# Performance work log

Measured on AMD Instinct MI355X. Metric: run time of the kernel, lower is better.

The kernel has to match this reference:

```python
import jax, jax.numpy as jnp
import numpy as np

HIDDEN = 512
HEADS = 8
HEAD_DIM = HIDDEN // HEADS
EPS_LN = 1e-5
EPS_ATTN = 1e-6


def setup_inputs() -> dict:
    key = jax.random.key(0)
    ks = jax.random.split(key, 12)
    B, S, N, D = 4, 12, 2048, HIDDEN
    s = 1.0 / np.sqrt(D)
    x = jax.random.normal(ks[0], (B, S, N, D), dtype=jnp.float32)
    Wq = jax.random.normal(ks[1], (D, D), dtype=jnp.float32) * s
    bq = jnp.zeros((D,), dtype=jnp.float32)
    Wk = jax.random.normal(ks[2], (D, D), dtype=jnp.float32) * s
    bk = jnp.zeros((D,), dtype=jnp.float32)
    Wv = jax.random.normal(ks[3], (D, D), dtype=jnp.float32) * s
    bv = jnp.zeros((D,), dtype=jnp.float32)
    Wo = jax.random.normal(ks[4], (D, D), dtype=jnp.float32) * s
    bo = jnp.zeros((D,), dtype=jnp.float32)
    ln_g = jnp.ones((D,), dtype=jnp.float32)
    ln_b = jnp.zeros((D,), dtype=jnp.float32)
    return {"x": x, "Wq": Wq, "bq": bq, "Wk": Wk, "bk": bk,
            "Wv": Wv, "bv": bv, "Wo": Wo, "bo": bo,
            "ln_g": ln_g, "ln_b": ln_b}


def _layer_norm(x, g, b):
    mu = jnp.mean(x, axis=-1, keepdims=True)
    var = jnp.var(x, axis=-1, keepdims=True)
    return (x - mu) * jax.lax.rsqrt(var + EPS_LN) * g + b


def reference(x, Wq, bq, Wk, bk, Wv, bv, Wo, bo, ln_g, ln_b):
    B, S, N, D = x.shape
    L = S * N  # flattened spatiotemporal tokens
    residual = x
    h = _layer_norm(x, ln_g, ln_b).reshape(B, L, D)
    # projections; [B, L, D] -> [B, H, L, hd]
    def split_heads(t):
        return t.reshape(B, L, HEADS, HEAD_DIM).transpose(0, 2, 1, 3)
    q = split_heads(h @ Wq.T + bq)
    k = split_heads(h @ Wk.T + bk)
    v = split_heads(h @ Wv.T + bv)
    # elu+1 feature map
    q = jax.nn.elu(q) + 1.0
    k = jax.nn.elu(k) + 1.0
    # kv outer product: [B, H, hd, hd]
    kv = jnp.einsum('bhld,bhle->bhde', k, v)
    out = jnp.einsum('bhld,bhde->bhle', q, kv)
    normalizer = jnp.einsum('bhld,bhd->bhl', q, k.sum(axis=2))
    out = out / (normalizer[..., None] + EPS_ATTN)
    out = out.transpose(0, 2, 1, 3).reshape(B, L, D)
    out = out @ Wo.T + bo
    out = out.reshape(B, S, N, D)
    return out + residual
```

## Files before the change

### kernel.cpp

```cpp
#include <hip/hip_runtime.h>
#include <hip/hip_bf16.h>
#include <stdint.h>

#define DDIM 512
#define NHEAD 8
#define BATCH 4
#define LTOK 24576
#define MROWS 98304
#define QKV_MBLK 384
#define KVCH 96
#define OG_MBLK 768
#define OG_MBLK_B 192
#define PTILE 4160

typedef __attribute__((ext_vector_type(8))) short short8;
typedef __attribute__((ext_vector_type(4))) float f32x4;

__device__ __forceinline__ float bf2f(unsigned short u) {
  union { unsigned int i; float f; } c; c.i = ((unsigned int)u) << 16; return c.f;
}
__device__ __forceinline__ unsigned short f2bf(float f) {
  __hip_bfloat16 h = __float2bfloat16(f);
  return __builtin_bit_cast(unsigned short, h);
}
__device__ __forceinline__ void gload16(const void* g, void* l) {
  __builtin_amdgcn_global_load_lds((const __attribute__((address_space(1))) void*)g,
                                   (__attribute__((address_space(3))) void*)l, 16, 0, 0);
}
__device__ __forceinline__ float elu1(float v) { return (v > 0.f) ? (v + 1.f) : __expf(v); }

__global__ __launch_bounds__(256) void wprep(const float* __restrict__ Wq, const float* __restrict__ bq,
                                             const float* __restrict__ Wk, const float* __restrict__ bk,
                                             const float* __restrict__ Wv, const float* __restrict__ bv,
                                             const float* __restrict__ Wo,
                                             unsigned short* __restrict__ wf,
                                             unsigned short* __restrict__ wob,
                                             float* __restrict__ biasf) {
  long t = (long)blockIdx.x * 256 + threadIdx.x;
  if (t < 786432) {
    int f = (int)(t >> 9), c = (int)(t & 511);
    const float* src;
    if (f < 1024) { int hh = f >> 7, kv = (f >> 6) & 1, d = f & 63;
                    src = (kv ? Wv : Wk) + (long)(hh * 64 + d) * 512; }
    else          src = Wq + (long)(f - 1024) * 512;
    wf[t] = f2bf(src[c]);
  } else if (t < 786432 + 262144) {
    long i = t - 786432; wob[i] = f2bf(Wo[i]);
  } else if (t < 786432 + 262144 + 1536) {
    int f = (int)(t - (786432 + 262144));
    float v;
    if (f < 1024) { int hh = f >> 7, kv = (f >> 6) & 1, d = f & 63; v = (kv ? bv : bk)[hh * 64 + d]; }
    else v = bq[f - 1024];
    biasf[f] = v;
  }
}

__global__ __launch_bounds__(256) void ln_kernel(const float* __restrict__ x,
                                                 const float* __restrict__ g,
                                                 const float* __restrict__ b,
                                                 unsigned short* __restrict__ h) {
  int wv = threadIdx.x >> 6, lane = threadIdx.x & 63;
  long row = (long)blockIdx.x * 4 + wv;
  const float* xr = x + row * DDIM + lane * 8;
  float4 v0 = *(const float4*)xr;
  float4 v1 = *(const float4*)(xr + 4);
  float s  = v0.x + v0.y + v0.z + v0.w + v1.x + v1.y + v1.z + v1.w;
  float s2 = v0.x*v0.x + v0.y*v0.y + v0.z*v0.z + v0.w*v0.w
           + v1.x*v1.x + v1.y*v1.y + v1.z*v1.z + v1.w*v1.w;
  #pragma unroll
  for (int o = 32; o; o >>= 1) { s += __shfl_xor(s, o); s2 += __shfl_xor(s2, o); }
  float mu = s * (1.0f / DDIM);
  float var = s2 * (1.0f / DDIM) - mu * mu;
  float rs = rsqrtf(var + 1e-5f);
  float4 g0 = *(const float4*)(g + lane * 8);
  float4 g1 = *(const float4*)(g + lane * 8 + 4);
  float4 b0 = *(const float4*)(b + lane * 8);
  float4 b1 = *(const float4*)(b + lane * 8 + 4);
  short8 o;
  o[0] = (short)f2bf((v0.x - mu) * rs * g0.x + b0.x);
  o[1] = (short)f2bf((v0.y - mu) * rs * g0.y + b0.y);
  o[2] = (short)f2bf((v0.z - mu) * rs * g0.z + b0.z);
  o[3] = (short)f2bf((v0.w - mu) * rs * g0.w + b0.w);
  o[4] = (short)f2bf((v1.x - mu) * rs * g1.x + b1.x);
  o[5] = (short)f2bf((v1.y - mu) * rs * g1.y + b1.y);
  o[6] = (short)f2bf((v1.z - mu) * rs * g1.z + b1.z);
  o[7] = (short)f2bf((v1.w - mu) * rs * g1.w + b1.w);
  *(short8*)(h + row * DDIM + lane * 8) = o;
}

__device__ __forceinline__ short8 ldsfrag(const unsigned short* h, int row, int kg) {
  return *(const short8*)&h[row * 32 + ((kg ^ ((row >> 1) & 3)) << 3)];
}

__device__ __forceinline__ void stage_half(const unsigned short* gbase,
                                           unsigned short* ldsbase, int tid) {
  #pragma unroll
  for (int i = 0; i < 2; i++) {
    int c = i * 512 + tid;
    int rr = c >> 2, cc = c & 3;
    int sc = ((cc ^ ((rr >> 1) & 3)) << 3);
    gload16(gbase + (long)rr * DDIM + sc, ldsbase + c * 8);
  }
}

template <int VMP1, int VMP3, bool S01, bool S23>
__device__ __forceinline__ void ktile(int t, unsigned short* lds,
                                      const unsigned short* Ab, const unsigned short* Wb,
                                      f32x4 (&acc)[8][4],
                                      int wm, int wn, int lr, int kg, int tid) {
  const int buf = t & 1;
  unsigned short* A0l = lds + (buf * 2 + 0) * 8192;
  unsigned short* A1l = lds + (buf * 2 + 1) * 8192;
  unsigned short* B0l = lds + 32768 + (buf * 2 + 0) * 8192;
  unsigned short* B1l = lds + 32768 + (buf * 2 + 1) * 8192;
  unsigned short* A1n = lds + ((buf ^ 1) * 2 + 1) * 8192;
  unsigned short* B1n = lds + 32768 + ((buf ^ 1) * 2 + 1) * 8192;
  short8 a[4], b[4];

  #pragma unroll
  for (int m = 0; m < 4; m++) a[m] = ldsfrag(A0l, wm * 128 + m * 16 + lr, kg);
  #pragma unroll
  for (int n = 0; n < 4; n++) b[n] = ldsfrag(B0l, wn * 64 + n * 16 + lr, kg);
  if (S01) stage_half(Ab + (long)(t + 1) * 64 + 32, A1n, tid);
  __builtin_amdgcn_s_barrier();
  __builtin_amdgcn_s_setprio(1);
  #pragma unroll
  for (int m = 0; m < 4; m++)
    #pragma unroll
    for (int n = 0; n < 4; n++)
      acc[m][n] = __builtin_amdgcn_mfma_f32_16x16x32_bf16(a[m], b[n], acc[m][n], 0, 0, 0);
  __builtin_amdgcn_s_setprio(0);
  __builtin_amdgcn_s_barrier();
  __builtin_amdgcn_sched_barrier(0);

  #pragma unroll
  for (int m = 0; m < 4; m++) a[m] = ldsfrag(A0l, wm * 128 + (4 + m) * 16 + lr, kg);
  if (S01) stage_half(Wb + (long)(t + 1) * 64 + 32, B1n, tid);
  __builtin_amdgcn_s_barrier();
  __builtin_amdgcn_s_setprio(1);
  #pragma unroll
  for (int m = 0; m < 4; m++)
    #pragma unroll
    for (int n = 0; n < 4; n++)
      acc[4 + m][n] = __builtin_amdgcn_mfma_f32_16x16x32_bf16(a[m], b[n], acc[4 + m][n], 0, 0, 0);
  __builtin_amdgcn_s_setprio(0);
  asm volatile("s_waitcnt vmcnt(%0)" :: "i"(VMP1) : "memory");
  __builtin_amdgcn_s_barrier();
  __builtin_amdgcn_sched_barrier(0);

  #pragma unroll
  for (int m = 0; m < 4; m++) a[m] = ldsfrag(A1l, wm * 128 + m * 16 + lr, kg);
  #pragma unroll
  for (int n = 0; n < 4; n++) b[n] = ldsfrag(B1l, wn * 64 + n * 16 + lr, kg);
  if (S23) stage_half(Ab + (long)(t + 2) * 64, A0l, tid);
  __builtin_amdgcn_s_barrier();
  __builtin_amdgcn_s_setprio(1);
  #pragma unroll
  for (int m = 0; m < 4; m++)
    #pragma unroll
    for (int n = 0; n < 4; n++)
      acc[m][n] = __builtin_amdgcn_mfma_f32_16x16x32_bf16(a[m], b[n], acc[m][n], 0, 0, 0);
  __builtin_amdgcn_s_setprio(0);
  __builtin_amdgcn_s_barrier();
  __builtin_amdgcn_sched_barrier(0);

  #pragma unroll
  for (int m = 0; m < 4; m++) a[m] = ldsfrag(A1l, wm * 128 + (4 + m) * 16 + lr, kg);
  if (S23) stage_half(Wb + (long)(t + 2) * 64, B0l, tid);
  __builtin_amdgcn_s_barrier();
  __builtin_amdgcn_s_setprio(1);
  #pragma unroll
  for (int m = 0; m < 4; m++)
    #pragma unroll
    for (int n = 0; n < 4; n++)
      acc[4 + m][n] = __builtin_amdgcn_mfma_f32_16x16x32_bf16(a[m], b[n], acc[4 + m][n], 0, 0, 0);
  __builtin_amdgcn_s_setprio(0);
  asm volatile("s_waitcnt vmcnt(%0)" :: "i"(VMP3) : "memory");
  __builtin_amdgcn_s_barrier();
  __builtin_amdgcn_sched_barrier(0);
}

__global__ __launch_bounds__(512, 2) void qkv_gemm(const unsigned short* __restrict__ A,
                                                   const unsigned short* __restrict__ wf,
                                                   const float* __restrict__ biasf,
                                                   unsigned short* __restrict__ qbuf,
                                                   unsigned short* __restrict__ part) {
  __shared__ unsigned short lds[65536];

  int tid = threadIdx.x;
  int wv = tid >> 6, lane = tid & 63;
  int wm = wv >> 2, wn = wv & 3;
  int kg = lane >> 4, lr = lane & 15;

  int lin = blockIdx.x;
  int g = lin / 48, r = lin % 48;
  int xb = g * 8 + (r & 7);
  int y  = r >> 3;
  long mBase = (long)xb * 256;
  int nBase = y * 256;

  const unsigned short* Ab = A + mBase * DDIM;
  const unsigned short* Wb = wf + (long)nBase * DDIM;

  f32x4 acc[8][4];
  #pragma unroll
  for (int m = 0; m < 8; m++)
    #pragma unroll
    for (int n = 0; n < 4; n++) acc[m][n] = (f32x4){0.f, 0.f, 0.f, 0.f};

  stage_half(Ab,       lds + 0 * 8192, tid);
  stage_half(Wb,       lds + 32768 + 0 * 8192, tid);
  stage_half(Ab + 32,  lds + 1 * 8192, tid);
  stage_half(Wb + 32,  lds + 32768 + 1 * 8192, tid);
  stage_half(Ab + 64,  lds + 2 * 8192, tid);
  stage_half(Wb + 64,  lds + 32768 + 2 * 8192, tid);
  asm volatile("s_waitcnt vmcnt(8)" ::: "memory");
  __builtin_amdgcn_s_barrier();
  __builtin_amdgcn_sched_barrier(0);

  #pragma unroll 1
  for (int i = 0; i < 3; i++) {
    ktile<8, 8, true, true>(2 * i,     lds, Ab, Wb, acc, wm, wn, lr, kg, tid);
    ktile<8, 8, true, true>(2 * i + 1, lds, Ab, Wb, acc, wm, wn, lr, kg, tid);
  }
  ktile<8, 4, true, false>(6, lds, Ab, Wb, acc, wm, wn, lr, kg, tid);
  ktile<0, 63, false, false>(7, lds, Ab, Wb, acc, wm, wn, lr, kg, tid);

  __syncthreads();

  if (y < 4) {
    unsigned short* kT = lds;
    unsigned short* vT = lds + 16896;
    int batch = xb / KVCH;
    int cIdx  = xb % KVCH;

    {
      int rr = 64 + (tid >> 5), cc = tid & 31;
      short8 z;
      #pragma unroll
      for (int j = 0; j < 8; j++) z[j] = (rr == 64) ? (short)0x3F80 : (short)0;
      *(short8*)&vT[rr * 264 + cc * 8] = z;
    }

    #pragma unroll 1
    for (int p = 0; p < 2; p++) {
      if ((wn >> 1) == p) {
        bool isV = wn & 1;
        #pragma unroll
        for (int n = 0; n < 4; n++) {
          int feat = n * 16 + lr;
          float bv = biasf[nBase + wn * 64 + n * 16 + lr];
          #pragma unroll
          for (int m = 0; m < 8; m++)
            #pragma unroll
            for (int j = 0; j < 4; j++) {
              int tok = wm * 128 + m * 16 + kg * 4 + j;
              float v = acc[m][n][j] + bv;
              if (!isV) kT[feat * 264 + tok] = f2bf(elu1(v));
              else      vT[feat * 264 + tok] = f2bf(v);
            }
        }
      }
      __syncthreads();

      int mt = wv & 3, ngrp = wv >> 2;
      int h = y * 2 + p;
      long pbase = ((long)(batch * 8 + h) * KVCH + cIdx) * PTILE;
      if (!ngrp) {
        f32x4 pa0 = {0,0,0,0}, pa1 = {0,0,0,0}, pa2 = {0,0,0,0};
        #pragma unroll
        for (int kk = 0; kk < 8; kk++) {
          short8 af = *(const short8*)&kT[(mt * 16 + lr) * 264 + kk * 32 + kg * 8];
          short8 b0 = *(const short8*)&vT[(0 * 16 + lr) * 264 + kk * 32 + kg * 8];
          short8 b1 = *(const short8*)&vT[(1 * 16 + lr) * 264 + kk * 32 + kg * 8];
          short8 b2 = *(const short8*)&vT[(2 * 16 + lr) * 264 + kk * 32 + kg * 8];
          pa0 = __builtin_amdgcn_mfma_f32_16x16x32_bf16(af, b0, pa0, 0, 0, 0);
          pa1 = __builtin_amdgcn_mfma_f32_16x16x32_bf16(af, b1, pa1, 0, 0, 0);
          pa2 = __builtin_amdgcn_mfma_f32_16x16x32_bf16(af, b2, pa2, 0, 0, 0);
        }
        #pragma unroll
        for (int j = 0; j < 4; j++) {
          int d = mt * 16 + kg * 4 + j;
          part[pbase + d * 64 + (0 * 16 + lr)] = f2bf(pa0[j]);
          part[pbase + d * 64 + (1 * 16 + lr)] = f2bf(pa1[j]);
          part[pbase + d * 64 + (2 * 16 + lr)] = f2bf(pa2[j]);
        }
      } else {
        f32x4 pa0 = {0,0,0,0}, pa1 = {0,0,0,0};
        #pragma unroll
        for (int kk = 0; kk < 8; kk++) {
          short8 af = *(const short8*)&kT[(mt * 16 + lr) * 264 + kk * 32 + kg * 8];
          short8 b0 = *(const short8*)&vT[(3 * 16 + lr) * 264 + kk * 32 + kg * 8];
          short8 b1 = *(const short8*)&vT[(4 * 16 + lr) * 264 + kk * 32 + kg * 8];
          pa0 = __builtin_amdgcn_mfma_f32_16x16x32_bf16(af, b0, pa0, 0, 0, 0);
          pa1 = __builtin_amdgcn_mfma_f32_16x16x32_bf16(af, b1, pa1, 0, 0, 0);
        }
        #pragma unroll
        for (int j = 0; j < 4; j++) {
          int d = mt * 16 + kg * 4 + j;
          part[pbase + d * 64 + (3 * 16 + lr)] = f2bf(pa0[j]);
          if (lr == 0) part[pbase + 4096 + d] = f2bf(pa1[j]);
        }
      }
      __syncthreads();
    }
  } else {
    unsigned short* Cs = lds;
    int qc0 = (y - 4) * 256;
    #pragma unroll 1
    for (int half = 0; half < 2; half++) {
      if (wm == half) {
        #pragma unroll
        for (int n = 0; n < 4; n++) {
          int col = wn * 64 + n * 16 + lr;
          float bv = biasf[nBase + col];
          #pragma unroll
          for (int m = 0; m < 8; m++)
            #pragma unroll
            for (int j = 0; j < 4; j++) {
              int rowl = m * 16 + kg * 4 + j;
              Cs[rowl * 264 + col] = f2bf(elu1(acc[m][n][j] + bv));
            }
        }
      }
      __syncthreads();
      #pragma unroll
      for (int i = 0; i < 8; i++) {
        int idx = i * 512 + tid;
        int row = idx >> 5, ch = idx & 31;
        *(short8*)&qbuf[(mBase + half * 128 + row) * DDIM + qc0 + ch * 8] =
            *(const short8*)&Cs[row * 264 + ch * 8];
      }
      __syncthreads();
    }
  }
}

__global__ __launch_bounds__(256) void kv_final(const unsigned short* __restrict__ part,
                                                unsigned short* __restrict__ kvD,
                                                float* __restrict__ ksum) {
  int bh = blockIdx.x;
  int idx = blockIdx.y * 256 + threadIdx.x;
  if (idx >= PTILE) return;
  const unsigned short* base = part + (long)bh * KVCH * PTILE + idx;
  float s = 0.f;
  for (int c = 0; c < KVCH; c++) s += bf2f(base[(long)c * PTILE]);
  if (idx < 4096) kvD[bh * 4096 + idx] = f2bf(s);
  else            ksum[bh * 64 + (idx - 4096)] = s;
}

__global__ __launch_bounds__(512) void w2_gemm(const unsigned short* __restrict__ kvD,
                                               const unsigned short* __restrict__ wob,
                                               unsigned short* __restrict__ Bmat) {
  __shared__ unsigned short W2s[512 * 72];
  int t = threadIdx.x, wv = t >> 6, lane = t & 63;
  int kg = lane >> 4, lr = lane & 15;
  int bh = blockIdx.x, b = bh >> 3, h = bh & 7;
  const unsigned short* kva = kvD + bh * 4096;

  short8 a[4][2];
  #pragma unroll
  for (int m = 0; m < 4; m++)
    #pragma unroll
    for (int kk = 0; kk < 2; kk++)
      a[m][kk] = *(const short8*)&kva[(m * 16 + lr) * 64 + kk * 32 + kg * 8];

  f32x4 acc[4][4];
  #pragma unroll
  for (int m = 0; m < 4; m++)
    #pragma unroll
    for (int n = 0; n < 4; n++) acc[m][n] = (f32x4){0.f, 0.f, 0.f, 0.f};

  #pragma unroll
  for (int n = 0; n < 4; n++) {
    int c = wv * 64 + n * 16 + lr;
    #pragma unroll
    for (int kk = 0; kk < 2; kk++) {
      short8 bfr = *(const short8*)&wob[(long)c * 512 + h * 64 + kk * 32 + kg * 8];
      #pragma unroll
      for (int m = 0; m < 4; m++)
        acc[m][n] = __builtin_amdgcn_mfma_f32_16x16x32_bf16(a[m][kk], bfr, acc[m][n], 0, 0, 0);
    }
  }
  #pragma unroll
  for (int m = 0; m < 4; m++)
    #pragma unroll
    for (int n = 0; n < 4; n++)
      #pragma unroll
      for (int j = 0; j < 4; j++)
        W2s[(wv * 64 + n * 16 + lr) * 72 + m * 16 + kg * 4 + j] = f2bf(acc[m][n][j]);
  __syncthreads();
  #pragma unroll
  for (int pp = 0; pp < 8; pp++) {
    int idx = pp * 512 + t;
    int c = idx >> 3, ch = (idx & 7) * 8;
    *(short8*)&Bmat[(long)b * 262144 + (long)c * 512 + h * 64 + ch] =
        *(const short8*)&W2s[c * 72 + ch];
  }
}

__global__ __launch_bounds__(256) void qscale(unsigned short* __restrict__ q,
                                              const float* __restrict__ ksum) {
  int wv = threadIdx.x >> 6, lane = threadIdx.x & 63;
  long row = (long)blockIdx.x * 4 + wv;
  int batch = (int)(row / LTOK);
  int bh = batch * 8 + (lane >> 3);
  unsigned short* qr = q + row * DDIM + lane * 8;
  short8 qv = *(const short8*)qr;
  const float* ks = ksum + bh * 64 + (lane & 7) * 8;
  float4 k0 = *(const float4*)ks;
  float4 k1 = *(const float4*)(ks + 4);
  float qf[8];
  #pragma unroll
  for (int j = 0; j < 8; j++) qf[j] = bf2f((unsigned short)qv[j]);
  float n = qf[0]*k0.x + qf[1]*k0.y + qf[2]*k0.z + qf[3]*k0.w
          + qf[4]*k1.x + qf[5]*k1.y + qf[6]*k1.z + qf[7]*k1.w;
  n += __shfl_xor(n, 1);
  n += __shfl_xor(n, 2);
  n += __shfl_xor(n, 4);
  float s = 1.0f / (n + 1e-6f);
  short8 o;
  #pragma unroll
  for (int j = 0; j < 8; j++) o[j] = (short)f2bf(qf[j] * s);
  *(short8*)qr = o;
}

__global__ __launch_bounds__(256) void ogemm(const unsigned short* __restrict__ A,
                                             const unsigned short* __restrict__ Bm,
                                             const float* __restrict__ bo,
                                             const float* __restrict__ xres,
                                             float* __restrict__ out) {
  __shared__ union {
    struct { unsigned short As[128 * 64]; unsigned short Bs[128 * 64]; } st;
    float Cs[64 * 132];
  } sm;

  int t = threadIdx.x;
  int wv = t >> 6, lane = t & 63;
  int wm = wv >> 1, wn = wv & 1;
  int kg = lane >> 4, lr = lane & 15;

  int lin = blockIdx.x;
  int g = lin >> 5, r = lin & 31;
  int xb = g * 8 + (r & 7);
  int y  = r >> 3;
  long mBase = (long)xb * 128;
  int nBase = y * 128;
  int batch = xb / OG_MBLK_B;

  f32x4 acc[4][4];
  #pragma unroll
  for (int m = 0; m < 4; m++)
    #pragma unroll
    for (int n = 0; n < 4; n++) acc[m][n] = (f32x4){0.f, 0.f, 0.f, 0.f};

  const unsigned short* Ab = A + mBase * DDIM;
  const unsigned short* Bb = Bm + (long)batch * 262144 + (long)nBase * DDIM;

  for (int k0 = 0; k0 < DDIM; k0 += 64) {
    #pragma unroll
    for (int i = 0; i < 4; i++) {
      int c = i * 256 + t;
      int rr = c >> 3, cc = c & 7;
      int sc = ((cc ^ (rr & 7)) << 3);
      gload16(Ab + (long)rr * DDIM + k0 + sc, sm.st.As + c * 8);
      gload16(Bb + (long)rr * DDIM + k0 + sc, sm.st.Bs + c * 8);
    }
    __syncthreads();
    #pragma unroll
    for (int kk = 0; kk < 2; kk++) {
      short8 a[4], b[4];
      #pragma unroll
      for (int m = 0; m < 4; m++) {
        int row = wm * 64 + m * 16 + lr;
        a[m] = *(const short8*)&sm.st.As[row * 64 + (((kk * 4 + kg) ^ (row & 7)) << 3)];
      }
      #pragma unroll
      for (int n = 0; n < 4; n++) {
        int row = wn * 64 + n * 16 + lr;
        b[n] = *(const short8*)&sm.st.Bs[row * 64 + (((kk * 4 + kg) ^ (row & 7)) << 3)];
      }
      #pragma unroll
      for (int m = 0; m < 4; m++)
        #pragma unroll
        for (int n = 0; n < 4; n++)
          acc[m][n] = __builtin_amdgcn_mfma_f32_16x16x32_bf16(a[m], b[n], acc[m][n], 0, 0, 0);
    }
    __syncthreads();
  }

  for (int p = 0; p < 2; p++) {
    __syncthreads();
    if (wm == p) {
      #pragma unroll
      for (int n = 0; n < 4; n++) {
        int col = wn * 64 + n * 16 + lr;
        float bv = bo[nBase + col];
        #pragma unroll
        for (int m = 0; m < 4; m++)
          #pragma unroll
          for (int j = 0; j < 4; j++) {
            int lrow = m * 16 + kg * 4 + j;
            sm.Cs[lrow * 132 + col] = acc[m][n][j] + bv;
          }
      }
    }
    __syncthreads();
    #pragma unroll
    for (int pp = 0; pp < 8; pp++) {
      int idx = pp * 256 + t;
      int row = idx >> 5, c4 = idx & 31;
      long goff = (mBase + p * 64 + row) * DDIM + nBase + c4 * 4;
      float4 rv = *(const float4*)&xres[goff];
      float4 cv = *(const float4*)&sm.Cs[row * 132 + c4 * 4];
      float4 ov; ov.x = cv.x + rv.x; ov.y = cv.y + rv.y; ov.z = cv.z + rv.z; ov.w = cv.w + rv.w;
      *(float4*)&out[goff] = ov;
    }
  }
}

extern "C" void kernel_launch(void* const* d_in, const int* in_sizes, int n_in,
                              void* d_out, int out_size, void* d_ws, size_t ws_size,
                              hipStream_t stream) {
  const float* x    = (const float*)d_in[0];
  const float* Wq   = (const float*)d_in[1];
  const float* bq   = (const float*)d_in[2];
  const float* Wk   = (const float*)d_in[3];
  const float* bk   = (const float*)d_in[4];
  const float* Wv   = (const float*)d_in[5];
  const float* bv   = (const float*)d_in[6];
  const float* Wo   = (const float*)d_in[7];
  const float* bo   = (const float*)d_in[8];
  const float* ln_g = (const float*)d_in[9];
  const float* ln_b = (const float*)d_in[10];

  char* ws = (char*)d_ws;
  size_t SZ = (size_t)MROWS * DDIM * 2;
  unsigned short* hbuf = (unsigned short*)ws;
  unsigned short* qbuf = (unsigned short*)(ws + SZ);
  char* p = ws + 2 * SZ;
  unsigned short* wf   = (unsigned short*)p;  p += (size_t)1536 * 512 * 2;
  unsigned short* wob  = (unsigned short*)p;  p += (size_t)512 * 512 * 2;
  float* biasf         = (float*)p;           p += 1536 * 4;
  p = (char*)(((uintptr_t)p + 255) & ~(uintptr_t)255);
  unsigned short* part = (unsigned short*)p;  p += (size_t)32 * KVCH * PTILE * 2;
  unsigned short* kvD  = (unsigned short*)p;  p += (size_t)32 * 4096 * 2;
  float* ksum          = (float*)p;           p += 32 * 64 * 4;
  p = (char*)(((uintptr_t)p + 255) & ~(uintptr_t)255);
  unsigned short* Bmat = (unsigned short*)p;  p += (size_t)BATCH * 512 * 512 * 2;

  wprep<<<(786432 + 262144 + 1536 + 255) / 256, 256, 0, stream>>>(Wq, bq, Wk, bk, Wv, bv, Wo,
                                                                  wf, wob, biasf);
  ln_kernel<<<MROWS / 4, 256, 0, stream>>>(x, ln_g, ln_b, hbuf);
  qkv_gemm<<<QKV_MBLK * 6, 512, 0, stream>>>(hbuf, wf, biasf, qbuf, part);
  kv_final<<<dim3(32, (PTILE + 255) / 256), 256, 0, stream>>>(part, kvD, ksum);
  w2_gemm<<<32, 512, 0, stream>>>(kvD, wob, Bmat);
  qscale<<<MROWS / 4, 256, 0, stream>>>(qbuf, ksum);
  ogemm<<<OG_MBLK * 4, 256, 0, stream>>>(qbuf, Bmat, bo, x, (float*)d_out);
}
```

Baseline: 505.2 us.

## Reuse pipelined 256x256 QKV k-loop for output GEMM and vectorize kv_final

Factors the software-pipelined 256x256 tile k-loop out of qkv_gemm and reuses it in the output projection, which moves from a simple 128x128 single-buffered loop to 512-thread blocks with 256x256 tiles. The epilogue now stages through LDS with an XOR swizzle in place of padding, and fuses bias and residual. kv_final now reads 8 bf16 values per thread with vector loads, cutting scalar memory transactions. This raises data reuse and overlap in the output GEMM, at the cost of fewer blocks (768) and higher register pressure.

```diff
diff --git a/kernel.cpp b/kernel.cpp
--- a/kernel.cpp
+++ b/kernel.cpp
@@ -9,8 +9,6 @@
 #define MROWS 98304
 #define QKV_MBLK 384
 #define KVCH 96
-#define OG_MBLK 768
-#define OG_MBLK_B 192
 #define PTILE 4160
 
 typedef __attribute__((ext_vector_type(8))) short short8;
@@ -180,34 +178,10 @@
   __builtin_amdgcn_sched_barrier(0);
 }
 
-__global__ __launch_bounds__(512, 2) void qkv_gemm(const unsigned short* __restrict__ A,
-                                                   const unsigned short* __restrict__ wf,
-                                                   const float* __restrict__ biasf,
-                                                   unsigned short* __restrict__ qbuf,
-                                                   unsigned short* __restrict__ part) {
-  __shared__ unsigned short lds[65536];
-
-  int tid = threadIdx.x;
-  int wv = tid >> 6, lane = tid & 63;
-  int wm = wv >> 2, wn = wv & 3;
-  int kg = lane >> 4, lr = lane & 15;
-
-  int lin = blockIdx.x;
-  int g = lin / 48, r = lin % 48;
-  int xb = g * 8 + (r & 7);
-  int y  = r >> 3;
-  long mBase = (long)xb * 256;
-  int nBase = y * 256;
-
-  const unsigned short* Ab = A + mBase * DDIM;
-  const unsigned short* Wb = wf + (long)nBase * DDIM;
-
-  f32x4 acc[8][4];
-  #pragma unroll
-  for (int m = 0; m < 8; m++)
-    #pragma unroll
-    for (int n = 0; n < 4; n++) acc[m][n] = (f32x4){0.f, 0.f, 0.f, 0.f};
-
+__device__ __forceinline__ void kloop256(unsigned short* lds,
+                                         const unsigned short* Ab, const unsigned short* Wb,
+                                         f32x4 (&acc)[8][4],
+                                         int wm, int wn, int lr, int kg, int tid) {
   stage_half(Ab,       lds + 0 * 8192, tid);
   stage_half(Wb,       lds + 32768 + 0 * 8192, tid);
   stage_half(Ab + 32,  lds + 1 * 8192, tid);
@@ -225,7 +199,37 @@
   }
   ktile<8, 4, true, false>(6, lds, Ab, Wb, acc, wm, wn, lr, kg, tid);
   ktile<0, 63, false, false>(7, lds, Ab, Wb, acc, wm, wn, lr, kg, tid);
-
+}
+
+__global__ __launch_bounds__(512, 2) void qkv_gemm(const unsigned short* __restrict__ A,
+                                                   const unsigned short* __restrict__ wf,
+                                                   const float* __restrict__ biasf,
+                                                   unsigned short* __restrict__ qbuf,
+                                                   unsigned short* __restrict__ part) {
+  __shared__ unsigned short lds[65536];
+
+  int tid = threadIdx.x;
+  int wv = tid >> 6, lane = tid & 63;
+  int wm = wv >> 2, wn = wv & 3;
+  int kg = lane >> 4, lr = lane & 15;
+
+  int lin = blockIdx.x;
+  int g = lin / 48, r = lin % 48;
+  int xb = g * 8 + (r & 7);
+  int y  = r >> 3;
+  long mBase = (long)xb * 256;
+  int nBase = y * 256;
+
+  const unsigned short* Ab = A + mBase * DDIM;
+  const unsigned short* Wb = wf + (long)nBase * DDIM;
+
+  f32x4 acc[8][4];
+  #pragma unroll
+  for (int m = 0; m < 8; m++)
+    #pragma unroll
+    for (int n = 0; n < 4; n++) acc[m][n] = (f32x4){0.f, 0.f, 0.f, 0.f};
+
+  kloop256(lds, Ab, Wb, acc, wm, wn, lr, kg, tid);
   __syncthreads();
 
   if (y < 4) {
@@ -340,13 +344,29 @@
                                                 unsigned short* __restrict__ kvD,
                                                 float* __restrict__ ksum) {
   int bh = blockIdx.x;
-  int idx = blockIdx.y * 256 + threadIdx.x;
-  if (idx >= PTILE) return;
-  const unsigned short* base = part + (long)bh * KVCH * PTILE + idx;
-  float s = 0.f;
-  for (int c = 0; c < KVCH; c++) s += bf2f(base[(long)c * PTILE]);
-  if (idx < 4096) kvD[bh * 4096 + idx] = f2bf(s);
-  else            ksum[bh * 64 + (idx - 4096)] = s;
+  int gidx = blockIdx.y * 256 + threadIdx.x;
+  if (gidx >= 520) return;
+  long idx0 = (long)gidx * 8;
+  const unsigned short* base = part + (long)bh * KVCH * PTILE + idx0;
+  float s[8];
+  #pragma unroll
+  for (int j = 0; j < 8; j++) s[j] = 0.f;
+  #pragma unroll 4
+  for (int c = 0; c < KVCH; c++) {
+    short8 v = *(const short8*)(base + (long)c * PTILE);
+    #pragma unroll
+    for (int j = 0; j < 8; j++) s[j] += bf2f((unsigned short)v[j]);
+  }
+  if (idx0 < 4096) {
+    short8 o;
+    #pragma unroll
+    for (int j = 0; j < 8; j++) o[j] = (short)f2bf(s[j]);
+    *(short8*)&kvD[bh * 4096 + idx0] = o;
+  } else {
+    int d0 = (int)(idx0 - 4096);
+    #pragma unroll
+    for (int j = 0; j < 8; j++) ksum[bh * 64 + d0 + j] = s[j];
+  }
 }
 
 __global__ __launch_bounds__(512) void w2_gemm(const unsigned short* __restrict__ kvD,
@@ -425,97 +445,68 @@
   *(short8*)qr = o;
 }
 
-__global__ __launch_bounds__(256) void ogemm(const unsigned short* __restrict__ A,
-                                             const unsigned short* __restrict__ Bm,
-                                             const float* __restrict__ bo,
-                                             const float* __restrict__ xres,
-                                             float* __restrict__ out) {
-  __shared__ union {
-    struct { unsigned short As[128 * 64]; unsigned short Bs[128 * 64]; } st;
-    float Cs[64 * 132];
-  } sm;
-
-  int t = threadIdx.x;
-  int wv = t >> 6, lane = t & 63;
-  int wm = wv >> 1, wn = wv & 1;
+__global__ __launch_bounds__(512, 2) void ogemm(const unsigned short* __restrict__ A,
+                                                const unsigned short* __restrict__ Bm,
+                                                const float* __restrict__ bo,
+                                                const float* __restrict__ xres,
+                                                float* __restrict__ out) {
+  __shared__ unsigned short lds[65536];
+
+  int tid = threadIdx.x;
+  int wv = tid >> 6, lane = tid & 63;
+  int wm = wv >> 2, wn = wv & 3;
   int kg = lane >> 4, lr = lane & 15;
 
   int lin = blockIdx.x;
-  int g = lin >> 5, r = lin & 31;
+  int g = lin >> 4, r = lin & 15;
   int xb = g * 8 + (r & 7);
   int y  = r >> 3;
-  long mBase = (long)xb * 128;
-  int nBase = y * 128;
-  int batch = xb / OG_MBLK_B;
-
-  f32x4 acc[4][4];
-  #pragma unroll
-  for (int m = 0; m < 4; m++)
+  long mBase = (long)xb * 256;
+  int nBase = y * 256;
+  int batch = xb / 96;
+
+  const unsigned short* Ab = A + mBase * DDIM;
+  const unsigned short* Wb = Bm + (long)batch * 262144 + (long)nBase * DDIM;
+
+  f32x4 acc[8][4];
+  #pragma unroll
+  for (int m = 0; m < 8; m++)
     #pragma unroll
     for (int n = 0; n < 4; n++) acc[m][n] = (f32x4){0.f, 0.f, 0.f, 0.f};
 
-  const unsigned short* Ab = A + mBase * DDIM;
-  const unsigned short* Bb = Bm + (long)batch * 262144 + (long)nBase * DDIM;
-
-  for (int k0 = 0; k0 < DDIM; k0 += 64) {
-    #pragma unroll
-    for (int i = 0; i < 4; i++) {
-      int c = i * 256 + t;
-      int rr = c >> 3, cc = c & 7;
-      int sc = ((cc ^ (rr & 7)) << 3);
-      gload16(Ab + (long)rr * DDIM + k0 + sc, sm.st.As + c * 8);
-      gload16(Bb + (long)rr * DDIM + k0 + sc, sm.st.Bs + c * 8);
-    }
-    __syncthreads();
-    #pragma unroll
-    for (int kk = 0; kk < 2; kk++) {
-      short8 a[4], b[4];
-      #pragma unroll
-      for (int m = 0; m < 4; m++) {
-        int row = wm * 64 + m * 16 + lr;
-        a[m] = *(const short8*)&sm.st.As[row * 64 + (((kk * 4 + kg) ^ (row & 7)) << 3)];
-      }
-      #pragma unroll
-      for (int n = 0; n < 4; n++) {
-        int row = wn * 64 + n * 16 + lr;
-        b[n] = *(const short8*)&sm.st.Bs[row * 64 + (((kk * 4 + kg) ^ (row & 7)) << 3)];
-      }
-      #pragma unroll
-      for (int m = 0; m < 4; m++)
-        #pragma unroll
-        for (int n = 0; n < 4; n++)
-          acc[m][n] = __builtin_amdgcn_mfma_f32_16x16x32_bf16(a[m], b[n], acc[m][n], 0, 0, 0);
-    }
-    __syncthreads();
-  }
-
-  for (int p = 0; p < 2; p++) {
-    __syncthreads();
-    if (wm == p) {
+  kloop256(lds, Ab, Wb, acc, wm, wn, lr, kg, tid);
+  __syncthreads();
+
+  float* Cs = (float*)lds;
+  #pragma unroll 1
+  for (int half = 0; half < 2; half++) {
+    if (wm == half) {
       #pragma unroll
       for (int n = 0; n < 4; n++) {
         int col = wn * 64 + n * 16 + lr;
         float bv = bo[nBase + col];
         #pragma unroll
-        for (int m = 0; m < 4; m++)
+        for (int m = 0; m < 8; m++)
           #pragma unroll
           for (int j = 0; j < 4; j++) {
             int lrow = m * 16 + kg * 4 + j;
-            sm.Cs[lrow * 132 + col] = acc[m][n][j] + bv;
+            Cs[lrow * 256 + (col ^ (((lrow >> 2) & 3) << 4))] = acc[m][n][j] + bv;
           }
       }
     }
     __syncthreads();
     #pragma unroll
-    for (int pp = 0; pp < 8; pp++) {
-      int idx = pp * 256 + t;
-      int row = idx >> 5, c4 = idx & 31;
-      long goff = (mBase + p * 64 + row) * DDIM + nBase + c4 * 4;
+    for (int it = 0; it < 16; it++) {
+      int idx = it * 512 + tid;
+      int row = idx >> 6, c4 = idx & 63;
+      int pcol = (c4 * 4) ^ (((row >> 2) & 3) << 4);
+      long goff = (mBase + half * 128 + row) * DDIM + nBase + c4 * 4;
       float4 rv = *(const float4*)&xres[goff];
-      float4 cv = *(const float4*)&sm.Cs[row * 132 + c4 * 4];
+      float4 cv = *(const float4*)&Cs[row * 256 + pcol];
       float4 ov; ov.x = cv.x + rv.x; ov.y = cv.y + rv.y; ov.z = cv.z + rv.z; ov.w = cv.w + rv.w;
       *(float4*)&out[goff] = ov;
     }
+    __syncthreads();
   }
 }
 
@@ -553,8 +544,8 @@
                                                                   wf, wob, biasf);
   ln_kernel<<<MROWS / 4, 256, 0, stream>>>(x, ln_g, ln_b, hbuf);
   qkv_gemm<<<QKV_MBLK * 6, 512, 0, stream>>>(hbuf, wf, biasf, qbuf, part);
-  kv_final<<<dim3(32, (PTILE + 255) / 256), 256, 0, stream>>>(part, kvD, ksum);
+  kv_final<<<dim3(32, 3), 256, 0, stream>>>(part, kvD, ksum);
   w2_gemm<<<32, 512, 0, stream>>>(kvD, wob, Bmat);
   qscale<<<MROWS / 4, 256, 0, stream>>>(qbuf, ksum);
-  ogemm<<<OG_MBLK * 4, 256, 0, stream>>>(qbuf, Bmat, bo, x, (float*)d_out);
-}
+  ogemm<<<QKV_MBLK * 2, 512, 0, stream>>>(qbuf, Bmat, bo, x, (float*)d_out);
+}
```

Result: faster. 492.8 us (-2.5%).
